# Optimization experiments

Measured on AMD Instinct MI355X. Metric: run time of the kernel, lower is better.

## Reference

```python
import jax, jax.numpy as jnp
import numpy as np

B, S, C = 1, 6, 128
Hf, Wf = 56, 100            # feature map (stride-8 of 448x800)
IMG_H, IMG_W = 448, 800
Z, Y, X = 128, 8, 128
BOUNDS = (-50.0, 50.0, -5.0, 5.0, -50.0, 50.0)
CENTROID = (0.0, 0.1, 0.0)
EPS = 1e-6


def _voxel_centers():
    # ref-frame (cam0) coordinates of voxel centers, Vox_util.Mem2Ref of gridcloud3d
    xmin, xmax = BOUNDS[0] + CENTROID[0], BOUNDS[1] + CENTROID[0]
    ymin, ymax = BOUNDS[2] + CENTROID[1], BOUNDS[3] + CENTROID[1]
    zmin, zmax = BOUNDS[4] + CENTROID[2], BOUNDS[5] + CENTROID[2]
    vsx, vsy, vsz = (xmax - xmin) / X, (ymax - ymin) / Y, (zmax - zmin) / Z
    zi, yi, xi = jnp.meshgrid(jnp.arange(Z), jnp.arange(Y), jnp.arange(X), indexing='ij')
    xr = xmin + vsx * 0.5 + xi.astype(jnp.float32) * vsx
    yr = ymin + vsy * 0.5 + yi.astype(jnp.float32) * vsy
    zr = zmin + vsz * 0.5 + zi.astype(jnp.float32) * vsz
    return jnp.stack([xr.reshape(-1), yr.reshape(-1), zr.reshape(-1)], axis=-1)  # (N,3), N=Z*Y*X


def setup_inputs() -> dict:
    key = jax.random.key(0)
    k1, k2 = jax.random.split(key)
    cam_feat = jax.random.normal(k1, (B, S, C, Hf, Wf), dtype=jnp.float32)
    # intrinsics: fx=fy=500, principal point at image center
    K = np.zeros((B, S, 4, 4), np.float32)
    K[..., 0, 0] = 500.0; K[..., 1, 1] = 500.0
    K[..., 0, 2] = IMG_W / 2.0; K[..., 1, 2] = IMG_H / 2.0
    K[..., 2, 2] = 1.0; K[..., 3, 3] = 1.0
    # surround-view rig: rotate about y (camera-frame vertical) by 2*pi*s/S
    ang = np.arange(S) * (2.0 * np.pi / S)
    c, s = np.cos(ang).astype(np.float32), np.sin(ang).astype(np.float32)
    R = np.zeros((B, S, 3, 3), np.float32)
    R[..., 0, 0] = c; R[..., 0, 2] = s; R[..., 1, 1] = 1.0
    R[..., 2, 0] = -s; R[..., 2, 2] = c
    t = np.stack([0.5 * s, np.full(S, -1.0, np.float32), 0.5 * c], axis=-1)[None].astype(np.float32)
    conv_w = jax.random.normal(k2, (C, C * Y, 3, 3), dtype=jnp.float32) * 0.02
    return {
        'cam_feat': cam_feat,
        'intrins': jnp.asarray(K),
        'rots': jnp.asarray(R),
        'trans': jnp.asarray(t),
        'conv_w': conv_w,
    }


def reference(cam_feat, intrins, rots, trans, conv_w):
    Bn, Sn = cam_feat.shape[:2]
    BS = Bn * Sn
    # velo_T_cams = [R|t]; cam0_T_camXs = inv(velo_T_cams[:,0]) @ velo_T_cams
    velo_T = (jnp.zeros((Bn, Sn, 4, 4), cam_feat.dtype)
              .at[..., :3, :3].set(rots)
              .at[..., :3, 3].set(trans)
              .at[..., 3, 3].set(1.0))
    cam0_T_camXs = jnp.einsum('bij,bsjk->bsik', jnp.linalg.inv(velo_T[:, 0]), velo_T)
    camXs_T_cam0 = jnp.linalg.inv(cam0_T_camXs)  # (B,S,4,4)
    # scale_intrinsics to feature resolution
    sx, sy = Wf / float(IMG_W), Hf / float(IMG_H)
    Kf = (jnp.zeros((Bn, Sn, 4, 4), cam_feat.dtype)
          .at[..., 0, 0].set(intrins[..., 0, 0] * sx)
          .at[..., 1, 1].set(intrins[..., 1, 1] * sy)
          .at[..., 0, 2].set(intrins[..., 0, 2] * sx)
          .at[..., 1, 2].set(intrins[..., 1, 2] * sy)
          .at[..., 2, 2].set(1.0).at[..., 3, 3].set(1.0))
    pixB_T_cam0 = jnp.einsum('bsij,bsjk->bsik', Kf, camXs_T_cam0).reshape(BS, 4, 4)
    camXs_T_cam0 = camXs_T_cam0.reshape(BS, 4, 4)

    xyz = _voxel_centers()                                   # (N,3)
    xyz1 = jnp.concatenate([xyz, jnp.ones((xyz.shape[0], 1), xyz.dtype)], axis=-1)  # (N,4)
    cam_pts = jnp.einsum('pij,nj->pni', camXs_T_cam0, xyz1)  # (BS,N,4)
    z = cam_pts[..., 2]
    pix = jnp.einsum('pij,nj->pni', pixB_T_cam0, xyz1)       # (BS,N,4)
    denom = jnp.maximum(pix[..., 2:3], EPS)
    x = pix[..., 0] / denom[..., 0]
    y = pix[..., 1] / denom[..., 0]
    valid = (x > -0.5) & (x < Wf - 0.5) & (y > -0.5) & (y < Hf - 0.5) & (z > 0.0)

    # normalize_grid2d + grid_sample(align_corners=False) unnormalization
    gx = jnp.clip(2.0 * x / (Wf - 1) - 1.0, -2.0, 2.0)
    gy = jnp.clip(2.0 * y / (Hf - 1) - 1.0, -2.0, 2.0)
    ux = ((gx + 1.0) * Wf - 1.0) * 0.5
    uy = ((gy + 1.0) * Hf - 1.0) * 0.5
    x0f, y0f = jnp.floor(ux), jnp.floor(uy)
    wx, wy = ux - x0f, uy - y0f
    x0i, y0i = x0f.astype(jnp.int32), y0f.astype(jnp.int32)

    feat = cam_feat.reshape(BS, C, Hf * Wf)

    def corner(xi, yi, w):
        inb = (xi >= 0) & (xi < Wf) & (yi >= 0) & (yi < Hf)  # zeros padding
        idx = jnp.clip(yi, 0, Hf - 1) * Wf + jnp.clip(xi, 0, Wf - 1)
        v = jnp.take_along_axis(feat, idx[:, None, :], axis=2)  # (BS,C,N)
        return v * (w * inb.astype(w.dtype))[:, None, :]

    vals = (corner(x0i, y0i, (1 - wx) * (1 - wy))
            + corner(x0i + 1, y0i, wx * (1 - wy))
            + corner(x0i, y0i + 1, (1 - wx) * wy)
            + corner(x0i + 1, y0i + 1, wx * wy))
    vals = vals * valid[:, None, :].astype(vals.dtype)
    feat_mems = vals.reshape(Bn, Sn, C, Z, Y, X)

    # reduce_masked_mean over cameras
    mask = (jnp.abs(feat_mems) > 0).astype(feat_mems.dtype)
    feat_mem = jnp.sum(feat_mems * mask, axis=1) / (EPS + jnp.sum(mask, axis=1))  # (B,C,Z,Y,X)

    # BEV compress: permute(0,1,3,2,4) -> (B, C*Y, Z, X), conv3x3 + InstanceNorm + GELU
    bev = jnp.transpose(feat_mem, (0, 1, 3, 2, 4)).reshape(Bn, C * Y, Z, X)
    out = jax.lax.conv_general_dilated(bev, conv_w, (1, 1), 'SAME',
                                       dimension_numbers=('NCHW', 'OIHW', 'NCHW'))
    mu = out.mean(axis=(2, 3), keepdims=True)
    var = out.var(axis=(2, 3), keepdims=True)
    out = (out - mu) * jax.lax.rsqrt(var + 1e-5)
    return jax.nn.gelu(out, approximate=False)
```

## Files before the change

kernel.cpp:

```cpp
#include <hip/hip_runtime.h>
#include <cmath>

#define SNUM 6
#define CNUM 128
#define HF 56
#define WF 100
#define HW (HF*WF)
#define ZN 128
#define YN 8
#define XN 128
#define NVOX (ZN*YN*XN)

typedef __attribute__((ext_vector_type(8))) short bf16x8;
typedef __attribute__((ext_vector_type(4))) float f32x4;
typedef __attribute__((ext_vector_type(4))) int   i32x4;

__device__ __forceinline__ unsigned short f2bf(float f) {
    unsigned u = __builtin_bit_cast(unsigned, f);
    unsigned r = (u + 0x7FFFu + ((u >> 16) & 1u)) >> 16;
    return (unsigned short)r;
}
__device__ __forceinline__ float bf2f(unsigned short h) {
    unsigned u = (unsigned)h << 16;
    return __builtin_bit_cast(float, u);
}

__global__ void k_setup(const float* __restrict__ intrins,
                        const float* __restrict__ rots,
                        const float* __restrict__ trans,
                        float* __restrict__ mats) {
    int s = threadIdx.x;
    if (s >= SNUM) return;
    float R0[9], Rs[9], t0[3], ts[3];
    for (int i = 0; i < 9; ++i) { R0[i] = rots[i]; Rs[i] = rots[s*9 + i]; }
    for (int i = 0; i < 3; ++i) { t0[i] = trans[i]; ts[i] = trans[s*3 + i]; }
    float M[3][4];
    float d0 = t0[0]-ts[0], d1 = t0[1]-ts[1], d2 = t0[2]-ts[2];
    for (int i = 0; i < 3; ++i) {
        for (int j = 0; j < 3; ++j)
            M[i][j] = Rs[0*3+i]*R0[0*3+j] + Rs[1*3+i]*R0[1*3+j] + Rs[2*3+i]*R0[2*3+j];
        M[i][3] = Rs[0*3+i]*d0 + Rs[1*3+i]*d1 + Rs[2*3+i]*d2;
    }
    const float sx = (float)WF/800.0f, sy = (float)HF/448.0f;
    float fx = intrins[s*16 + 0]*sx, fy = intrins[s*16 + 5]*sy;
    float cx = intrins[s*16 + 2]*sx, cy = intrins[s*16 + 6]*sy;
    float* o = mats + s*24;
    for (int j = 0; j < 4; ++j) {
        o[0*4+j]      = M[0][j];
        o[1*4+j]      = M[1][j];
        o[2*4+j]      = M[2][j];
        o[12 + 0*4+j] = fx*M[0][j] + cx*M[2][j];
        o[12 + 1*4+j] = fy*M[1][j] + cy*M[2][j];
        o[12 + 2*4+j] = M[2][j];
    }
}

__global__ __launch_bounds__(256) void k_tfeat(const float* __restrict__ cf,
                                               unsigned short* __restrict__ featT) {
    __shared__ float t[32][33];
    int s = blockIdx.z;
    int p0 = blockIdx.x * 32, c0 = blockIdx.y * 32;
    int tx = threadIdx.x, ty = threadIdx.y;
#pragma unroll
    for (int k = 0; k < 4; ++k) {
        int r = ty + k*8;
        t[r][tx] = cf[((size_t)s*CNUM + c0 + r)*HW + p0 + tx];
    }
    __syncthreads();
#pragma unroll
    for (int k = 0; k < 4; ++k) {
        int r = ty + k*8;
        featT[((size_t)s*HW + p0 + r)*CNUM + c0 + tx] = f2bf(t[tx][r]);
    }
}

__global__ __launch_bounds__(256) void k_geo(const float* __restrict__ mats,
                                             float* __restrict__ uv) {
#pragma clang fp contract(off)
    int n = blockIdx.x * 256 + threadIdx.x;
    int zi = n >> 10, yi = (n >> 7) & 7, xi = n & 127;
    float xr = -49.609375f + (float)xi * 0.78125f;
    float yr = (-4.9f + 0.625f) + (float)yi * 1.25f;
    float zr = -49.609375f + (float)zi * 0.78125f;
#pragma unroll
    for (int s = 0; s < SNUM; ++s) {
        const float* m = mats + s*24;
        float zc = m[8]*xr  + m[9]*yr  + m[10]*zr + m[11];
        float ph = m[12]*xr + m[13]*yr + m[14]*zr + m[15];
        float qh = m[16]*xr + m[17]*yr + m[18]*zr + m[19];
        float denom = fmaxf(zc, 1e-6f);
        float px = ph / denom, py = qh / denom;
        bool valid = (px > -0.5f) & (px < (float)WF - 0.5f) &
                     (py > -0.5f) & (py < (float)HF - 0.5f) & (zc > 0.0f);
        float ux = -10000.0f, uy = -10000.0f;
        if (valid) {
            float gx = 2.0f*px/((float)WF - 1.0f) - 1.0f;
            float gy = 2.0f*py/((float)HF - 1.0f) - 1.0f;
            gx = fminf(fmaxf(gx, -2.0f), 2.0f);
            gy = fminf(fmaxf(gy, -2.0f), 2.0f);
            ux = ((gx + 1.0f)*(float)WF - 1.0f)*0.5f;
            uy = ((gy + 1.0f)*(float)HF - 1.0f)*0.5f;
        }
        uv[(n*SNUM + s)*2]     = ux;
        uv[(n*SNUM + s)*2 + 1] = uy;
    }
}

__global__ __launch_bounds__(256) void k_sample(const unsigned short* __restrict__ featT,
                                                const float* __restrict__ uv,
                                                unsigned short* __restrict__ bevin) {
#pragma clang fp contract(off)
    __shared__ float xch[16][132];
    const int tid = threadIdx.x;
    const int b = blockIdx.x;
    const int z = b >> 6, x0 = (b & 63) * 2;
    const int cl = tid & 15, vs = tid >> 4;
    const int y = vs >> 1, xs = vs & 1;
    const int n = z*1024 + y*128 + x0 + xs;
    const bf16x8 zz8 = {0,0,0,0,0,0,0,0};
    float sum[8], cnt[8];
#pragma unroll
    for (int k = 0; k < 8; ++k) { sum[k] = 0.0f; cnt[k] = 0.0f; }
    for (int s = 0; s < SNUM; ++s) {
        float2 u = ((const float2*)uv)[n*SNUM + s];
        if (u.x < -999.0f) continue;
        float x0f = floorf(u.x), y0f = floorf(u.y);
        float wx = u.x - x0f, wy = u.y - y0f;
        int ix = (int)x0f, iy = (int)y0f;
        float w00 = (1.0f-wx)*(1.0f-wy), w10 = wx*(1.0f-wy);
        float w01 = (1.0f-wx)*wy,        w11 = wx*wy;
        bool bx0 = (ix >= 0) & (ix < WF);
        bool bx1 = (ix >= -1) & (ix < WF-1);
        bool by0 = (iy >= 0) & (iy < HF);
        bool by1 = (iy >= -1) & (iy < HF-1);
        bool c00 = bx0 & by0, c10 = bx1 & by0, c01 = bx0 & by1, c11 = bx1 & by1;
        const unsigned short* fb = featT + (size_t)s * (HW*CNUM) + cl*8;
        long r0 = (long)(iy*WF + ix) * CNUM;
        bf16x8 v00 = c00 ? *(const bf16x8*)(fb + r0)                 : zz8;
        bf16x8 v10 = c10 ? *(const bf16x8*)(fb + r0 + CNUM)          : zz8;
        bf16x8 v01 = c01 ? *(const bf16x8*)(fb + r0 + WF*CNUM)       : zz8;
        bf16x8 v11 = c11 ? *(const bf16x8*)(fb + r0 + WF*CNUM + CNUM): zz8;
#pragma unroll
        for (int k = 0; k < 8; ++k) {
            float v = 0.0f;
            v = v + w00 * bf2f((unsigned short)v00[k]);
            v = v + w10 * bf2f((unsigned short)v10[k]);
            v = v + w01 * bf2f((unsigned short)v01[k]);
            v = v + w11 * bf2f((unsigned short)v11[k]);
            sum[k] += v;
            cnt[k] += (v != 0.0f) ? 1.0f : 0.0f;
        }
    }
#pragma unroll
    for (int k = 0; k < 8; ++k)
        xch[vs][cl*8 + k] = sum[k] / (1e-6f + cnt[k]);
    __syncthreads();
#pragma unroll
    for (int j = 0; j < 4; ++j) {
        int m = tid + j*256;
        int xs2 = m >> 9;
        int r = m & 511;
        int c = (2*r) >> 3, y0 = (2*r) & 7;
        float v0 = xch[y0*2 + xs2][c];
        float v1 = xch[(y0+1)*2 + xs2][c];
        unsigned pk = (unsigned)f2bf(v0) | ((unsigned)f2bf(v1) << 16);
        ((unsigned*)bevin)[(size_t)(z*128 + x0 + xs2)*512 + r] = pk;
    }
}

__global__ __launch_bounds__(256) void k_wprep(const float* __restrict__ w,
                                               unsigned short* __restrict__ w2) {
    int i = blockIdx.x*256 + threadIdx.x;
    if (i >= 9*128*1024) return;
    int ci = i & 1023; int rest = i >> 10; int co = rest & 127; int tap = rest >> 7;
    w2[i] = f2bf(w[((size_t)co*1024 + ci)*9 + tap]);
}

__global__ __launch_bounds__(256, 1) void k_conv_mfma(
        const unsigned short* __restrict__ bevin,
        const unsigned short* __restrict__ w2,
        float* __restrict__ out) {
    __shared__ unsigned short lds[2][12*130*8];
    const int tid  = threadIdx.x;
    const int z0   = blockIdx.x;
    const int coh  = blockIdx.y;
    const int lane = tid & 63, wid = tid >> 6;
    const int wr = wid >> 1, wx = wid & 1;
    const int co_base = coh*64 + wr*32;
    const int l15 = lane & 15, lhi = lane >> 4;

    if (tid < 48) {
        int bf = tid & 1, q = tid >> 1;
        int row = q >> 1, side = q & 1;
        *(i32x4*)&lds[bf][(row*130 + side*129)*8] = i32x4{0,0,0,0};
    }

    f32x4 acc[2][4];
#pragma unroll
    for (int f = 0; f < 2; ++f)
#pragma unroll
        for (int nf = 0; nf < 4; ++nf) acc[f][nf] = f32x4{0.f,0.f,0.f,0.f};

    const unsigned short* aw0 = w2 + ((size_t)(co_base      + l15))*1024 + lhi*8;
    const unsigned short* aw1 = w2 + ((size_t)(co_base + 16 + l15))*1024 + lhi*8;

    bf16x8 afr0[18], afr1[18];
    i32x4 pre[6];
    bool  pv[6];

#define A_LOAD(DST, CI0)                                                       \
    {                                                                          \
        _Pragma("unroll")                                                      \
        for (int t = 0; t < 9; ++t) {                                          \
            DST[t*2]   = *(const bf16x8*)(aw0 + (size_t)t*131072 + (CI0));     \
            DST[t*2+1] = *(const bf16x8*)(aw1 + (size_t)t*131072 + (CI0));     \
        }                                                                      \
    }
#define B_LOAD(CI0)                                                            \
    {                                                                          \
        _Pragma("unroll")                                                      \
        for (int j = 0; j < 6; ++j) {                                          \
            int i  = tid + j*256;                                              \
            int kg = i & 3, x = (i >> 2) & 127, zr = i >> 9;                   \
            int zz = z0 - 1 + zr;                                              \
            pv[j] = ((unsigned)zz < 128u);                                     \
            if (pv[j])                                                         \
                pre[j] = *(const i32x4*)&bevin[((size_t)(zz*128 + x))*1024 + (CI0) + kg*8]; \
        }                                                                      \
    }
#define B_WRITE(BUF)                                                           \
    {                                                                          \
        _Pragma("unroll")                                                      \
        for (int j = 0; j < 6; ++j) {                                          \
            int i  = tid + j*256;                                              \
            int kg = i & 3, x = (i >> 2) & 127, zr = i >> 9;                   \
            if (pv[j])                                                         \
                *(i32x4*)&lds[BUF][(((zr*4 + kg)*130) + 1 + x)*8] = pre[j];    \
        }                                                                      \
    }
#define COMPUTE(BUF, AFR)                                                      \
    {                                                                          \
        _Pragma("unroll")                                                      \
        for (int dz = 0; dz < 3; ++dz) {                                       \
            if ((unsigned)(z0 - 1 + dz) < 128u) {                              \
                _Pragma("unroll")                                              \
                for (int dx = 0; dx < 3; ++dx) {                               \
                    bf16x8 a0 = AFR[(dz*3+dx)*2];                              \
                    bf16x8 a1 = AFR[(dz*3+dx)*2+1];                            \
                    _Pragma("unroll")                                          \
                    for (int nf = 0; nf < 4; ++nf) {                           \
                        int xp = wx*64 + nf*16 + l15 + dx;                     \
                        bf16x8 bfr = *(const bf16x8*)&lds[BUF][(((dz*4 + lhi)*130) + xp)*8]; \
                        acc[0][nf] = __builtin_amdgcn_mfma_f32_16x16x32_bf16(a0, bfr, acc[0][nf], 0, 0, 0); \
                        acc[1][nf] = __builtin_amdgcn_mfma_f32_16x16x32_bf16(a1, bfr, acc[1][nf], 0, 0, 0); \
                    }                                                          \
                }                                                              \
            }                                                                  \
        }                                                                      \
    }

    B_LOAD(0);
    A_LOAD(afr0, 0);
    __syncthreads();
    B_WRITE(0);
    __syncthreads();

    for (int cc = 0; cc < 16; ++cc) {
        const int ci0 = cc*64;
        B_LOAD(ci0 + 32);
        A_LOAD(afr1, ci0 + 32);
        COMPUTE(0, afr0);
        B_WRITE(1);
        __syncthreads();
        if (cc < 15) {
            B_LOAD(ci0 + 64);
            A_LOAD(afr0, ci0 + 64);
        }
        COMPUTE(1, afr1);
        if (cc < 15) {
            B_WRITE(0);
            __syncthreads();
        }
    }

#pragma unroll
    for (int f = 0; f < 2; ++f)
#pragma unroll
        for (int nf = 0; nf < 4; ++nf)
#pragma unroll
            for (int r = 0; r < 4; ++r) {
                int co = co_base + f*16 + lhi*4 + r;
                out[(size_t)co*16384 + z0*128 + wx*64 + nf*16 + l15] = acc[f][nf][r];
            }
#undef A_LOAD
#undef B_LOAD
#undef B_WRITE
#undef COMPUTE
}

__global__ __launch_bounds__(256) void k_instnorm_stats(const float* __restrict__ out,
                                                        float* __restrict__ stats) {
    __shared__ float r1[256], r2[256];
    int co = blockIdx.x, tid = threadIdx.x;
    const float* p = out + (size_t)co*16384;
    float s1 = 0.0f, s2 = 0.0f;
    for (int i = tid; i < 16384; i += 256) { float v = p[i]; s1 += v; s2 += v*v; }
    r1[tid] = s1; r2[tid] = s2;
    __syncthreads();
    for (int off = 128; off > 0; off >>= 1) {
        if (tid < off) { r1[tid] += r1[tid+off]; r2[tid] += r2[tid+off]; }
        __syncthreads();
    }
    if (tid == 0) {
        float mean = r1[0] * (1.0f/16384.0f);
        float var  = r2[0] * (1.0f/16384.0f) - mean*mean;
        stats[co*2]   = mean;
        stats[co*2+1] = rsqrtf(var + 1e-5f);
    }
}

__global__ __launch_bounds__(256) void k_gelu(float* __restrict__ out,
                                              const float* __restrict__ stats) {
    int i = blockIdx.x*256 + threadIdx.x;
    int co = i >> 14;
    float v = out[i];
    float r = (v - stats[co*2]) * stats[co*2+1];
    out[i] = 0.5f * r * (1.0f + erff(r * 0.70710678118654752f));
}

extern "C" void kernel_launch(void* const* d_in, const int* in_sizes, int n_in,
                              void* d_out, int out_size, void* d_ws, size_t ws_size,
                              hipStream_t stream) {
    const float* cam_feat = (const float*)d_in[0];
    const float* intrins  = (const float*)d_in[1];
    const float* rots     = (const float*)d_in[2];
    const float* trans    = (const float*)d_in[3];
    const float* conv_w   = (const float*)d_in[4];
    float* out = (float*)d_out;
    float* ws  = (float*)d_ws;

    float* mats  = ws;
    float* uv    = ws + 160;
    unsigned short* featT = (unsigned short*)(uv + (size_t)NVOX*12);
    unsigned short* bevin = featT + (size_t)SNUM*HW*CNUM;
    unsigned short* w2    = bevin + (size_t)16384*1024;
    float* stats = (float*)(w2 + 9*128*1024);

    hipLaunchKernelGGL(k_setup, dim3(1), dim3(64), 0, stream, intrins, rots, trans, mats);
    hipLaunchKernelGGL(k_tfeat, dim3(HW/32, CNUM/32, SNUM), dim3(32,8), 0, stream, cam_feat, featT);
    hipLaunchKernelGGL(k_geo, dim3(NVOX/256), dim3(256), 0, stream, mats, uv);
    hipLaunchKernelGGL(k_wprep, dim3((9*128*1024 + 255)/256), dim3(256), 0, stream, conv_w, w2);
    hipLaunchKernelGGL(k_sample, dim3(8192), dim3(256), 0, stream, featT, uv, bevin);
    hipLaunchKernelGGL(k_conv_mfma, dim3(128, 2), dim3(256), 0, stream, bevin, w2, out);
    hipLaunchKernelGGL(k_instnorm_stats, dim3(128), dim3(256), 0, stream, out, stats);
    hipLaunchKernelGGL(k_gelu, dim3(8192), dim3(256), 0, stream, out, stats);
}
```

Baseline: 157.1 us.

## Pad BEV input layout and stage conv tiles via direct global-to-LDS loads

After: 155.7 us. Within noise of the previous version (-0.8%).

```diff
diff --git a/kernel.cpp b/kernel.cpp
--- a/kernel.cpp
+++ b/kernel.cpp
@@ -23,6 +23,17 @@
 __device__ __forceinline__ float bf2f(unsigned short h) {
     unsigned u = (unsigned)h << 16;
     return __builtin_bit_cast(float, u);
+}
+
+__device__ __forceinline__ void gl_lds16(const void* g, void* l) {
+    __builtin_amdgcn_global_load_lds(
+        (const __attribute__((address_space(1))) void*)g,
+        (__attribute__((address_space(3))) void*)l, 16, 0, 0);
+}
+__device__ __forceinline__ void gl_lds4(const void* g, void* l) {
+    __builtin_amdgcn_global_load_lds(
+        (const __attribute__((address_space(1))) void*)g,
+        (__attribute__((address_space(3))) void*)l, 4, 0, 0);
 }
 
 __global__ void k_setup(const float* __restrict__ intrins,
@@ -106,9 +117,28 @@
     }
 }
 
+__global__ __launch_bounds__(256) void k_zero(unsigned short* __restrict__ bevin2) {
+    int i = blockIdx.x*256 + threadIdx.x;
+    if (i >= 66048) return;
+    size_t unit;
+    if (i < 33280) {
+        int zr = i / 16640;
+        int j  = i - zr*16640;
+        unit = (size_t)(zr ? 129 : 0)*16640 + j;
+    } else {
+        int j  = i - 33280;
+        int zp = 1 + (j >> 8);
+        int r  = j & 255;
+        int c  = r >> 1;
+        int xp = (r & 1) ? 129 : 0;
+        unit = ((size_t)zp*128 + c)*130 + xp;
+    }
+    *(i32x4*)&bevin2[unit*8] = i32x4{0,0,0,0};
+}
+
 __global__ __launch_bounds__(256) void k_sample(const unsigned short* __restrict__ featT,
                                                 const float* __restrict__ uv,
-                                                unsigned short* __restrict__ bevin) {
+                                                unsigned short* __restrict__ bevin2) {
 #pragma clang fp contract(off)
     __shared__ float xch[16][132];
     const int tid = threadIdx.x;
@@ -155,16 +185,17 @@
     for (int k = 0; k < 8; ++k)
         xch[vs][cl*8 + k] = sum[k] / (1e-6f + cnt[k]);
     __syncthreads();
-#pragma unroll
-    for (int j = 0; j < 4; ++j) {
-        int m = tid + j*256;
-        int xs2 = m >> 9;
-        int r = m & 511;
-        int c = (2*r) >> 3, y0 = (2*r) & 7;
-        float v0 = xch[y0*2 + xs2][c];
-        float v1 = xch[(y0+1)*2 + xs2][c];
-        unsigned pk = (unsigned)f2bf(v0) | ((unsigned)f2bf(v1) << 16);
-        ((unsigned*)bevin)[(size_t)(z*128 + x0 + xs2)*512 + r] = pk;
+    {
+        int c = tid >> 1, xs2 = tid & 1;
+        unsigned pk[4];
+#pragma unroll
+        for (int j = 0; j < 4; ++j) {
+            float v0 = xch[(2*j)*2 + xs2][c];
+            float v1 = xch[(2*j+1)*2 + xs2][c];
+            pk[j] = (unsigned)f2bf(v0) | ((unsigned)f2bf(v1) << 16);
+        }
+        size_t unit = ((size_t)(z+1)*128 + c)*130 + (x0 + xs2 + 1);
+        *(i32x4*)&bevin2[unit*8] = i32x4{(int)pk[0], (int)pk[1], (int)pk[2], (int)pk[3]};
     }
 }
 
@@ -176,25 +207,19 @@
     w2[i] = f2bf(w[((size_t)co*1024 + ci)*9 + tap]);
 }
 
-__global__ __launch_bounds__(256, 1) void k_conv_mfma(
-        const unsigned short* __restrict__ bevin,
+__global__ __launch_bounds__(128, 1) void k_conv_mfma(
+        const unsigned short* __restrict__ bevin2,
         const unsigned short* __restrict__ w2,
         float* __restrict__ out) {
-    __shared__ unsigned short lds[2][12*130*8];
+    __shared__ __align__(16) unsigned short lds[2][12*80*8];
     const int tid  = threadIdx.x;
     const int z0   = blockIdx.x;
-    const int coh  = blockIdx.y;
-    const int lane = tid & 63, wid = tid >> 6;
-    const int wr = wid >> 1, wx = wid & 1;
+    const int coh  = blockIdx.y >> 1;
+    const int xh   = blockIdx.y & 1;
+    const int lane = tid & 63, wr = tid >> 6;
     const int co_base = coh*64 + wr*32;
     const int l15 = lane & 15, lhi = lane >> 4;
 
-    if (tid < 48) {
-        int bf = tid & 1, q = tid >> 1;
-        int row = q >> 1, side = q & 1;
-        *(i32x4*)&lds[bf][(row*130 + side*129)*8] = i32x4{0,0,0,0};
-    }
-
     f32x4 acc[2][4];
 #pragma unroll
     for (int f = 0; f < 2; ++f)
@@ -205,9 +230,20 @@
     const unsigned short* aw1 = w2 + ((size_t)(co_base + 16 + l15))*1024 + lhi*8;
 
     bf16x8 afr0[18], afr1[18];
-    i32x4 pre[6];
-    bool  pv[6];
-
+
+#define STAGE(BUF, C0)                                                         \
+    {                                                                          \
+        _Pragma("unroll")                                                      \
+        for (int r6 = 0; r6 < 6; ++r6) {                                       \
+            int r = wr*6 + r6;                                                 \
+            int dzr = r >> 2, cg = r & 3;                                      \
+            const unsigned short* gsrc = bevin2 +                              \
+                (((size_t)(z0 + dzr)*128 + (C0) + cg)*130 + xh*64)*8;          \
+            unsigned short* ldst = &lds[BUF][r*80*8];                          \
+            gl_lds16(gsrc + (size_t)lane*8, ldst);                             \
+            gl_lds4 (gsrc + 64*8 + (size_t)lane*2, ldst + 64*8);               \
+        }                                                                      \
+    }
 #define A_LOAD(DST, CI0)                                                       \
     {                                                                          \
         _Pragma("unroll")                                                      \
@@ -216,71 +252,42 @@
             DST[t*2+1] = *(const bf16x8*)(aw1 + (size_t)t*131072 + (CI0));     \
         }                                                                      \
     }
-#define B_LOAD(CI0)                                                            \
-    {                                                                          \
-        _Pragma("unroll")                                                      \
-        for (int j = 0; j < 6; ++j) {                                          \
-            int i  = tid + j*256;                                              \
-            int kg = i & 3, x = (i >> 2) & 127, zr = i >> 9;                   \
-            int zz = z0 - 1 + zr;                                              \
-            pv[j] = ((unsigned)zz < 128u);                                     \
-            if (pv[j])                                                         \
-                pre[j] = *(const i32x4*)&bevin[((size_t)(zz*128 + x))*1024 + (CI0) + kg*8]; \
-        }                                                                      \
-    }
-#define B_WRITE(BUF)                                                           \
-    {                                                                          \
-        _Pragma("unroll")                                                      \
-        for (int j = 0; j < 6; ++j) {                                          \
-            int i  = tid + j*256;                                              \
-            int kg = i & 3, x = (i >> 2) & 127, zr = i >> 9;                   \
-            if (pv[j])                                                         \
-                *(i32x4*)&lds[BUF][(((zr*4 + kg)*130) + 1 + x)*8] = pre[j];    \
-        }                                                                      \
-    }
 #define COMPUTE(BUF, AFR)                                                      \
     {                                                                          \
+        __builtin_amdgcn_s_setprio(1);                                         \
         _Pragma("unroll")                                                      \
         for (int dz = 0; dz < 3; ++dz) {                                       \
-            if ((unsigned)(z0 - 1 + dz) < 128u) {                              \
+            _Pragma("unroll")                                                  \
+            for (int dx = 0; dx < 3; ++dx) {                                   \
+                bf16x8 a0 = AFR[(dz*3+dx)*2];                                  \
+                bf16x8 a1 = AFR[(dz*3+dx)*2+1];                                \
                 _Pragma("unroll")                                              \
-                for (int dx = 0; dx < 3; ++dx) {                               \
-                    bf16x8 a0 = AFR[(dz*3+dx)*2];                              \
-                    bf16x8 a1 = AFR[(dz*3+dx)*2+1];                            \
-                    _Pragma("unroll")                                          \
-                    for (int nf = 0; nf < 4; ++nf) {                           \
-                        int xp = wx*64 + nf*16 + l15 + dx;                     \
-                        bf16x8 bfr = *(const bf16x8*)&lds[BUF][(((dz*4 + lhi)*130) + xp)*8]; \
-                        acc[0][nf] = __builtin_amdgcn_mfma_f32_16x16x32_bf16(a0, bfr, acc[0][nf], 0, 0, 0); \
-                        acc[1][nf] = __builtin_amdgcn_mfma_f32_16x16x32_bf16(a1, bfr, acc[1][nf], 0, 0, 0); \
-                    }                                                          \
+                for (int nf = 0; nf < 4; ++nf) {                               \
+                    bf16x8 bfr = *(const bf16x8*)&lds[BUF][((dz*4 + lhi)*80 + nf*16 + l15 + dx)*8]; \
+                    acc[0][nf] = __builtin_amdgcn_mfma_f32_16x16x32_bf16(a0, bfr, acc[0][nf], 0, 0, 0); \
+                    acc[1][nf] = __builtin_amdgcn_mfma_f32_16x16x32_bf16(a1, bfr, acc[1][nf], 0, 0, 0); \
                 }                                                              \
             }                                                                  \
         }                                                                      \
-    }
-
-    B_LOAD(0);
+        __builtin_amdgcn_s_setprio(0);                                         \
+    }
+
+    STAGE(0, 0);
     A_LOAD(afr0, 0);
     __syncthreads();
-    B_WRITE(0);
-    __syncthreads();
 
     for (int cc = 0; cc < 16; ++cc) {
-        const int ci0 = cc*64;
-        B_LOAD(ci0 + 32);
-        A_LOAD(afr1, ci0 + 32);
+        const int k0 = 2*cc;
+        STAGE(1, (k0+1)*4);
+        A_LOAD(afr1, (k0+1)*32);
         COMPUTE(0, afr0);
-        B_WRITE(1);
         __syncthreads();
         if (cc < 15) {
-            B_LOAD(ci0 + 64);
-            A_LOAD(afr0, ci0 + 64);
+            STAGE(0, (k0+2)*4);
+            A_LOAD(afr0, (k0+2)*32);
         }
         COMPUTE(1, afr1);
-        if (cc < 15) {
-            B_WRITE(0);
-            __syncthreads();
-        }
+        if (cc < 15) __syncthreads();
     }
 
 #pragma unroll
@@ -290,11 +297,10 @@
 #pragma unroll
             for (int r = 0; r < 4; ++r) {
                 int co = co_base + f*16 + lhi*4 + r;
-                out[(size_t)co*16384 + z0*128 + wx*64 + nf*16 + l15] = acc[f][nf][r];
+                out[(size_t)co*16384 + z0*128 + xh*64 + nf*16 + l15] = acc[f][nf][r];
             }
+#undef STAGE
 #undef A_LOAD
-#undef B_LOAD
-#undef B_WRITE
 #undef COMPUTE
 }
 
@@ -341,17 +347,18 @@
 
     float* mats  = ws;
     float* uv    = ws + 160;
-    unsigned short* featT = (unsigned short*)(uv + (size_t)NVOX*12);
-    unsigned short* bevin = featT + (size_t)SNUM*HW*CNUM;
-    unsigned short* w2    = bevin + (size_t)16384*1024;
+    unsigned short* featT  = (unsigned short*)(uv + (size_t)NVOX*12);
+    unsigned short* bevin2 = featT + (size_t)SNUM*HW*CNUM;
+    unsigned short* w2     = bevin2 + (size_t)130*128*130*8;
     float* stats = (float*)(w2 + 9*128*1024);
 
     hipLaunchKernelGGL(k_setup, dim3(1), dim3(64), 0, stream, intrins, rots, trans, mats);
     hipLaunchKernelGGL(k_tfeat, dim3(HW/32, CNUM/32, SNUM), dim3(32,8), 0, stream, cam_feat, featT);
     hipLaunchKernelGGL(k_geo, dim3(NVOX/256), dim3(256), 0, stream, mats, uv);
     hipLaunchKernelGGL(k_wprep, dim3((9*128*1024 + 255)/256), dim3(256), 0, stream, conv_w, w2);
-    hipLaunchKernelGGL(k_sample, dim3(8192), dim3(256), 0, stream, featT, uv, bevin);
-    hipLaunchKernelGGL(k_conv_mfma, dim3(128, 2), dim3(256), 0, stream, bevin, w2, out);
+    hipLaunchKernelGGL(k_zero, dim3((66048 + 255)/256), dim3(256), 0, stream, bevin2);
+    hipLaunchKernelGGL(k_sample, dim3(8192), dim3(256), 0, stream, featT, uv, bevin2);
+    hipLaunchKernelGGL(k_conv_mfma, dim3(128, 4), dim3(128), 0, stream, bevin2, w2, out);
     hipLaunchKernelGGL(k_instnorm_stats, dim3(128), dim3(256), 0, stream, out, stats);
     hipLaunchKernelGGL(k_gelu, dim3(8192), dim3(256), 0, stream, out, stats);
 }
```
